# Optimization experiments

Measured on AMD Instinct MI355X. Metric: run time of the kernel, lower is better.

The kernel has to match this reference:

```python
import jax, jax.numpy as jnp
import numpy as np

NEG_SLOPE = 0.2
EPS = 1e-16  # matches PyG softmax epsilon


def gat_conv(x, src, dst, W, att_src, att_dst, bias):
    """PyG-style GATConv (concat heads, self-loops already in src/dst).
    x: [N, F_in]; W: [F_in, H*C]; att_*: [H, C]; bias: [H*C]."""
    N = x.shape[0]
    H, C = att_src.shape
    h = (x @ W).reshape(N, H, C)                       # [N,H,C]
    a_src = jnp.einsum('nhc,hc->nh', h, att_src)       # [N,H]
    a_dst = jnp.einsum('nhc,hc->nh', h, att_dst)
    e = jax.nn.leaky_relu(a_src[src] + a_dst[dst], NEG_SLOPE)   # [E,H]
    # segment softmax over incoming edges of each dst node
    e_max = jax.ops.segment_max(e, dst, num_segments=N)         # [N,H]
    e_max = jnp.where(jnp.isfinite(e_max), e_max, 0.0)
    e_exp = jnp.exp(e - e_max[dst])                              # [E,H]
    denom = jax.ops.segment_sum(e_exp, dst, num_segments=N)     # [N,H]
    alpha = e_exp / (denom[dst] + EPS)                           # [E,H]
    msg = h[src] * alpha[:, :, None]                             # [E,H,C]
    out = jax.ops.segment_sum(msg, dst, num_segments=N)         # [N,H,C]
    return out.reshape(N, H * C) + bias


def setup_inputs() -> dict:
    key = jax.random.key(0)
    ks = jax.random.split(key, 16)
    N, E = 50000, 800000
    F_in, C, H = 1280, 32, 8
    HC = H * C
    NG = 64  # graphs in batch
    x = jax.random.normal(ks[0], (N, F_in), dtype=jnp.float32)
    edge_index = jax.random.randint(ks[1], (2, E), 0, N, dtype=jnp.int64)
    batch = jnp.sort(jax.random.randint(ks[2], (N,), 0, NG, dtype=jnp.int64))
    s = 1.0 / np.sqrt(F_in)
    W1 = jax.random.normal(ks[3], (F_in, HC), dtype=jnp.float32) * s
    as1 = jax.random.normal(ks[4], (H, C), dtype=jnp.float32) * 0.1
    ad1 = jax.random.normal(ks[5], (H, C), dtype=jnp.float32) * 0.1
    b1 = jnp.zeros((HC,), dtype=jnp.float32)
    s2 = 1.0 / np.sqrt(HC)
    W2 = jax.random.normal(ks[6], (HC, HC), dtype=jnp.float32) * s2
    as2 = jax.random.normal(ks[7], (H, C), dtype=jnp.float32) * 0.1
    ad2 = jax.random.normal(ks[8], (H, C), dtype=jnp.float32) * 0.1
    b2 = jnp.zeros((HC,), dtype=jnp.float32)
    lin1_w = jax.random.normal(ks[9], (HC, 128), dtype=jnp.float32) * s2
    lin1_b = jnp.zeros((128,), dtype=jnp.float32)
    lin2_w = jax.random.normal(ks[10], (128, 1), dtype=jnp.float32) * (1.0 / np.sqrt(128))
    lin2_b = jnp.zeros((1,), dtype=jnp.float32)
    return {"x": x, "edge_index": edge_index, "batch": batch,
            "W1": W1, "as1": as1, "ad1": ad1, "b1": b1,
            "W2": W2, "as2": as2, "ad2": ad2, "b2": b2,
            "lin1_w": lin1_w, "lin1_b": lin1_b, "lin2_w": lin2_w, "lin2_b": lin2_b}


def reference(x, edge_index, batch, W1, as1, ad1, b1, W2, as2, ad2, b2,
              lin1_w, lin1_b, lin2_w, lin2_b):
    N = x.shape[0]
    NG = 64
    loops = jnp.arange(N, dtype=edge_index.dtype)
    src = jnp.concatenate([edge_index[0], loops])  # add self-loops (PyG default)
    dst = jnp.concatenate([edge_index[1], loops])
    h = jax.nn.relu(gat_conv(x, src, dst, W1, as1, ad1, b1))
    h = jax.nn.relu(gat_conv(h, src, dst, W2, as2, ad2, b2))
    # global mean pool over graphs
    sums = jax.ops.segment_sum(h, batch, num_segments=NG)               # [NG,HC]
    cnts = jax.ops.segment_sum(jnp.ones((N, 1), h.dtype), batch, num_segments=NG)
    pooled = sums / jnp.maximum(cnts, 1.0)
    z = jax.nn.relu(pooled @ lin1_w + lin1_b)
    out = z @ lin2_w + lin2_b                                            # [NG,1]
    return out.squeeze(-1)
```

## Files before the change

### kernel.cpp

```cpp
#include <hip/hip_runtime.h>
#include <hip/hip_bf16.h>
#include <math.h>

#define HC 256
#define NH 8
#define NEG_SLOPE 0.2f
#define CHW 64
#define LDA 136
#define MR 32
#define EL 264

typedef unsigned short u16;
typedef __attribute__((ext_vector_type(8))) short bf16x8;
typedef __attribute__((ext_vector_type(4))) float f32x4;

__device__ __forceinline__ u16 f2bf(float f) {
    unsigned int u = __float_as_uint(f);
    u += 0x7FFFu + ((u >> 16) & 1u);
    return (u16)(u >> 16);
}
__device__ __forceinline__ float bf2f(u16 s) {
    return __uint_as_float(((unsigned int)s) << 16);
}
__device__ __forceinline__ f32x4 bf4f(ushort4 v) {
    f32x4 r;
    r[0] = bf2f(v.x); r[1] = bf2f(v.y); r[2] = bf2f(v.z); r[3] = bf2f(v.w);
    return r;
}

#define BAR_LDS()                                                  \
    do {                                                           \
        asm volatile("s_waitcnt lgkmcnt(0)" ::: "memory");         \
        __builtin_amdgcn_s_barrier();                              \
        __builtin_amdgcn_sched_barrier(0);                         \
    } while (0)

__global__ __launch_bounds__(256) void pack_b_split(const float* __restrict__ B, int K,
                                                    u16* __restrict__ Bh,
                                                    u16* __restrict__ Bl) {
    const int g = blockIdx.x * 256 + threadIdx.x;
    const int lane = g & 63;
    const int f = (g >> 6) & 15;
    const int kt = g >> 10;
    const int col = f * 16 + (lane & 15);
    const int k0 = kt * 32 + (lane >> 4) * 8;
    bf16x8 hv, lv;
#pragma unroll
    for (int e = 0; e < 8; e++) {
        const float v = B[(size_t)(k0 + e) * HC + col];
        const u16 h = f2bf(v);
        hv[e] = (short)h;
        lv[e] = (short)f2bf(v - bf2f(h));
    }
    const size_t off = (size_t)g * 8;
    *(bf16x8*)(Bh + off) = hv;
    *(bf16x8*)(Bl + off) = lv;
}

template <typename AT>
__global__ __launch_bounds__(256) void gemm_fused(
    const AT* __restrict__ A,
    const u16* __restrict__ Bh, const u16* __restrict__ Bl,
    const float* __restrict__ att_s, const float* __restrict__ att_d,
    u16* __restrict__ h_out, float* __restrict__ a_src, float* __restrict__ a_dst,
    int M, int K) {
    __shared__ u16 ldsA[2][MR * LDA];
    const int tid = threadIdx.x;
    const int wid = tid >> 6;
    const int lane = tid & 63;
    const int rowblk = blockIdx.x;
    const int NG4 = K >> 7;
    const int rot = rowblk % NG4;

    f32x4 acc[2][4];
#pragma unroll
    for (int i = 0; i < 2; i++)
#pragma unroll
        for (int j = 0; j < 4; j++) acc[i][j] = (f32x4)0.f;

    const int srow = tid >> 3;
    const int scc = (tid & 7) * 16;
    const int grow = rowblk * MR + srow;
    const AT* aptr = (grow < M) ? (A + (size_t)grow * K + scc) : nullptr;
    const int woff = srow * LDA + scc;

    float4 pf[4];
    uint4 pu[2];
    auto loadAg = [&](int gg) {
        if constexpr (sizeof(AT) == 4) {
#pragma unroll
            for (int q = 0; q < 4; q++) {
                pf[q] = make_float4(0.f, 0.f, 0.f, 0.f);
                if (aptr) pf[q] = *(const float4*)((const float*)aptr + gg * 128 + q * 4);
            }
        } else {
            pu[0] = make_uint4(0, 0, 0, 0);
            pu[1] = make_uint4(0, 0, 0, 0);
            if (aptr) {
                pu[0] = *(const uint4*)((const u16*)aptr + gg * 128);
                pu[1] = *(const uint4*)((const u16*)aptr + gg * 128 + 8);
            }
        }
    };
    auto stageg = [&](int buf) {
        if constexpr (sizeof(AT) == 4) {
#pragma unroll
            for (int p = 0; p < 2; p++) {
                const float vv[8] = {pf[2 * p].x,     pf[2 * p].y,
                                     pf[2 * p].z,     pf[2 * p].w,
                                     pf[2 * p + 1].x, pf[2 * p + 1].y,
                                     pf[2 * p + 1].z, pf[2 * p + 1].w};
                bf16x8 hv;
#pragma unroll
                for (int e = 0; e < 8; e++) hv[e] = (short)f2bf(vv[e]);
                *(bf16x8*)&ldsA[buf][woff + p * 8] = hv;
            }
        } else {
            *(uint4*)&ldsA[buf][woff] = pu[0];
            *(uint4*)&ldsA[buf][woff + 8] = pu[1];
        }
    };
    auto readA = [&](int buf, int kk, bf16x8* ah) {
#pragma unroll
        for (int i = 0; i < 2; i++)
            ah[i] = *(const bf16x8*)&ldsA[buf][(i * 16 + (lane & 15)) * LDA +
                                              kk * 32 + (lane >> 4) * 8];
    };
    auto loadB = [&](int kt, bf16x8* bh, bf16x8* bl) {
        const u16* bHp = Bh + ((size_t)kt * 16 + wid * 4) * 512 + lane * 8;
        const u16* bLp = Bl + ((size_t)kt * 16 + wid * 4) * 512 + lane * 8;
#pragma unroll
        for (int j = 0; j < 4; j++) {
            bh[j] = *(const bf16x8*)(bHp + j * 512);
            bl[j] = *(const bf16x8*)(bLp + j * 512);
        }
    };
    auto mfma_tile = [&](const bf16x8* ah, const bf16x8* bh, const bf16x8* bl) {
#pragma unroll
        for (int i = 0; i < 2; i++)
#pragma unroll
            for (int j = 0; j < 4; j++) {
                acc[i][j] = __builtin_amdgcn_mfma_f32_16x16x32_bf16(ah[i], bh[j], acc[i][j], 0, 0, 0);
                acc[i][j] = __builtin_amdgcn_mfma_f32_16x16x32_bf16(ah[i], bl[j], acc[i][j], 0, 0, 0);
            }
    };

    loadAg(rot);
    stageg(0);
    if (NG4 > 1) loadAg((rot + 1) % NG4);
    BAR_LDS();

    bf16x8 bh[4], bl[4];
    int cur = 0;
    for (int g = 0; g < NG4; ++g) {
        const int gg = (g + rot) % NG4;
        if (g + 1 < NG4) stageg(cur ^ 1);
        if (g + 2 < NG4) loadAg((g + 2 + rot) % NG4);

        const int kt0 = gg * 4;
#pragma unroll
        for (int kk = 0; kk < 4; kk++) {
            loadB(kt0 + kk, bh, bl);
            bf16x8 ah[2];
            readA(cur, kk, ah);
            mfma_tile(ah, bh, bl);
        }
        BAR_LDS();
        cur ^= 1;
    }

    const int r0 = rowblk * MR;
    const int colb = wid * 64 + (lane & 15);
    float asw[4], adw[4];
#pragma unroll
    for (int j = 0; j < 4; j++) {
        asw[j] = att_s[colb + j * 16];
        adw[j] = att_d[colb + j * 16];
    }
#pragma unroll
    for (int i = 0; i < 2; i++) {
#pragma unroll
        for (int r = 0; r < 4; r++) {
            const int row = r0 + i * 16 + (lane >> 4) * 4 + r;
            float ps0 = acc[i][0][r] * asw[0] + acc[i][1][r] * asw[1];
            float ps1 = acc[i][2][r] * asw[2] + acc[i][3][r] * asw[3];
            float pd0 = acc[i][0][r] * adw[0] + acc[i][1][r] * adw[1];
            float pd1 = acc[i][2][r] * adw[2] + acc[i][3][r] * adw[3];
#pragma unroll
            for (int m = 1; m <= 8; m <<= 1) {
                ps0 += __shfl_xor(ps0, m);
                ps1 += __shfl_xor(ps1, m);
                pd0 += __shfl_xor(pd0, m);
                pd1 += __shfl_xor(pd1, m);
            }
            if (row < M && (lane & 15) == 0) {
                a_src[row * NH + 2 * wid + 0] = ps0;
                a_src[row * NH + 2 * wid + 1] = ps1;
                a_dst[row * NH + 2 * wid + 0] = pd0;
                a_dst[row * NH + 2 * wid + 1] = pd1;
            }
        }
    }

    u16* eps = &ldsA[0][0];
#pragma unroll
    for (int i = 0; i < 2; i++)
#pragma unroll
        for (int r = 0; r < 4; r++) {
            const int lrow = i * 16 + (lane >> 4) * 4 + r;
#pragma unroll
            for (int j = 0; j < 4; j++)
                eps[lrow * EL + colb + j * 16] = f2bf(acc[i][j][r]);
        }
    BAR_LDS();
#pragma unroll
    for (int q = 0; q < 4; q++) {
        const int t = q * 256 + tid;
        const int lrow = t >> 5;
        const int c8 = (t & 31) * 8;
        const bf16x8 v = *(const bf16x8*)&eps[lrow * EL + c8];
        const int growr = r0 + lrow;
        if (growr < M) *(bf16x8*)&h_out[(size_t)growr * HC + c8] = v;
    }
}

__global__ void count_deg(const int* __restrict__ dst, int E, int ET, int* __restrict__ deg) {
    const int e = blockIdx.x * blockDim.x + threadIdx.x;
    if (e >= ET) return;
    const int d = (e < E) ? dst[e] : (e - E);
    atomicAdd(&deg[d], 1);
}

__global__ __launch_bounds__(256) void scan_block(const int* __restrict__ deg,
                                                  int* __restrict__ row_ptr,
                                                  int* __restrict__ partials, int N) {
    __shared__ int sd[256];
    const int tid = threadIdx.x;
    const int base = blockIdx.x * 1024 + tid * 4;
    int v0 = (base + 0 < N) ? deg[base + 0] : 0;
    int v1 = (base + 1 < N) ? deg[base + 1] : 0;
    int v2 = (base + 2 < N) ? deg[base + 2] : 0;
    int v3 = (base + 3 < N) ? deg[base + 3] : 0;
    const int tsum = v0 + v1 + v2 + v3;
    sd[tid] = tsum;
    __syncthreads();
    int run = tsum;
    for (int off = 1; off < 256; off <<= 1) {
        int t = 0;
        if (tid >= off) t = sd[tid - off];
        __syncthreads();
        run += t;
        sd[tid] = run;
        __syncthreads();
    }
    const int excl = run - tsum;
    int s0 = excl + v0, s1 = s0 + v1, s2 = s1 + v2, s3 = s2 + v3;
    if (base + 0 < N) row_ptr[base + 1] = s0;
    if (base + 1 < N) row_ptr[base + 2] = s1;
    if (base + 2 < N) row_ptr[base + 3] = s2;
    if (base + 3 < N) row_ptr[base + 4] = s3;
    if (tid == 255) partials[blockIdx.x] = run;
}

__global__ __launch_bounds__(1024) void scan_partials(int* __restrict__ partials, int nb) {
    __shared__ int sd[1024];
    const int tid = threadIdx.x;
    int v = (tid < nb) ? partials[tid] : 0;
    sd[tid] = v;
    __syncthreads();
    int run = v;
    for (int off = 1; off < 1024; off <<= 1) {
        int t = 0;
        if (tid >= off) t = sd[tid - off];
        __syncthreads();
        run += t;
        sd[tid] = run;
        __syncthreads();
    }
    if (tid < nb) partials[tid] = run - v;
}

__global__ __launch_bounds__(256) void scan_add(int* __restrict__ row_ptr,
                                                const int* __restrict__ partials, int N) {
    const int i = blockIdx.x * 256 + threadIdx.x;
    if (i == 0) row_ptr[0] = 0;
    if (i < N) row_ptr[i + 1] += partials[i >> 10];
}

__global__ void scatter_edges(const int* __restrict__ src_in, const int* __restrict__ dst,
                              int E, int ET, const int* __restrict__ row_ptr,
                              int* __restrict__ cursor, int* __restrict__ esrc) {
    const int e = blockIdx.x * blockDim.x + threadIdx.x;
    if (e >= ET) return;
    const int d = (e < E) ? dst[e] : (e - E);
    const int s = (e < E) ? src_in[e] : (e - E);
    const int pos = atomicAdd(&cursor[d], 1);
    esrc[row_ptr[d] + pos] = s;
}

template <typename OT>
__global__ __launch_bounds__(256) void gat_aggregate_wave(
    const u16* __restrict__ h_bf, const float* __restrict__ a_src,
    const float* __restrict__ a_dst, const int* __restrict__ row_ptr,
    const int* __restrict__ esrc, const float* __restrict__ bias,
    OT* __restrict__ out, int N) {
    __shared__ int   s_src[4][CHW];
    __shared__ float s_ev[4][CHW][NH];

    const int tid = threadIdx.x;
    const int wv = tid >> 6;
    const int lane = tid & 63;
    const int n = blockIdx.x * 4 + wv;
    if (n >= N) return;

    const int beg = row_ptr[n];
    const int deg = row_ptr[n + 1] - beg;
    const int jj = lane >> 3;
    const int hh = lane & 7;
    const int g4 = lane >> 3;

    const float adh = a_dst[n * NH + hh];
    float m_run = -1e30f, d_run = 0.f;
    f32x4 acc = (f32x4)0.f;

    for (int c0 = 0; c0 < deg; c0 += CHW) {
        const int chlen = min(CHW, deg - c0);

        float lmax = -1e30f;
        for (int p = 0; p < chlen; p += 8) {
            const int j = p + jj;
            if (j < chlen) {
                const int s = esrc[beg + c0 + j];
                if (hh == 0) s_src[wv][j] = s;
                float v = a_src[s * NH + hh] + adh;
                v = (v > 0.f) ? v : NEG_SLOPE * v;
                s_ev[wv][j][hh] = v;
                lmax = fmaxf(lmax, v);
            }
        }
        lmax = fmaxf(lmax, __shfl_xor(lmax, 8));
        lmax = fmaxf(lmax, __shfl_xor(lmax, 16));
        lmax = fmaxf(lmax, __shfl_xor(lmax, 32));
        const float mo = m_run;
        const float mn = fmaxf(mo, lmax);
        const float scl = __expf(mo - mn);
        m_run = mn;

        float lsum = 0.f;
        for (int p = 0; p < chlen; p += 8) {
            const int j = p + jj;
            if (j < chlen) {
                const float pv = __expf(s_ev[wv][j][hh] - mn);
                s_ev[wv][j][hh] = pv;
                lsum += pv;
            }
        }
        lsum += __shfl_xor(lsum, 8);
        lsum += __shfl_xor(lsum, 16);
        lsum += __shfl_xor(lsum, 32);
        d_run = d_run * scl + lsum;

        __asm__ volatile("s_waitcnt lgkmcnt(0)" ::: "memory");

        const float scl4 = __shfl(scl, g4);
        f32x4 t0 = (f32x4)0.f, t1 = (f32x4)0.f, t2 = (f32x4)0.f, t3 = (f32x4)0.f;
        int j = 0;
        for (; j + 4 <= chlen; j += 4) {
            const int s0 = s_src[wv][j],     s1 = s_src[wv][j + 1];
            const int s2 = s_src[wv][j + 2], s3 = s_src[wv][j + 3];
            const float p0 = s_ev[wv][j][g4],     p1 = s_ev[wv][j + 1][g4];
            const float p2 = s_ev[wv][j + 2][g4], p3 = s_ev[wv][j + 3][g4];
            const f32x4 h0 = bf4f(*(const ushort4*)&h_bf[(size_t)s0 * HC + lane * 4]);
            const f32x4 h1 = bf4f(*(const ushort4*)&h_bf[(size_t)s1 * HC + lane * 4]);
            const f32x4 h2 = bf4f(*(const ushort4*)&h_bf[(size_t)s2 * HC + lane * 4]);
            const f32x4 h3 = bf4f(*(const ushort4*)&h_bf[(size_t)s3 * HC + lane * 4]);
#pragma unroll
            for (int q = 0; q < 4; q++) {
                t0[q] += p0 * h0[q];
                t1[q] += p1 * h1[q];
                t2[q] += p2 * h2[q];
                t3[q] += p3 * h3[q];
            }
        }
        for (; j < chlen; j++) {
            const int s0 = s_src[wv][j];
            const float p0 = s_ev[wv][j][g4];
            const f32x4 h0 = bf4f(*(const ushort4*)&h_bf[(size_t)s0 * HC + lane * 4]);
#pragma unroll
            for (int q = 0; q < 4; q++) t0[q] += p0 * h0[q];
        }
#pragma unroll
        for (int q = 0; q < 4; q++)
            acc[q] = acc[q] * scl4 + ((t0[q] + t1[q]) + (t2[q] + t3[q]));
    }

    const float invd = 1.f / (__shfl(d_run, g4) + 1e-16f);
    const f32x4 bv = *(const f32x4*)&bias[lane * 4];
    if constexpr (sizeof(OT) == 2) {
        ushort4 o4;
        o4.x = f2bf(fmaxf(acc[0] * invd + bv[0], 0.f));
        o4.y = f2bf(fmaxf(acc[1] * invd + bv[1], 0.f));
        o4.z = f2bf(fmaxf(acc[2] * invd + bv[2], 0.f));
        o4.w = f2bf(fmaxf(acc[3] * invd + bv[3], 0.f));
        *(ushort4*)&out[(size_t)n * HC + lane * 4] = o4;
    } else {
        f32x4 o;
#pragma unroll
        for (int q = 0; q < 4; q++) o[q] = fmaxf(acc[q] * invd + bv[q], 0.f);
        *(f32x4*)&out[(size_t)n * HC + lane * 4] = o;
    }
}

__global__ __launch_bounds__(256) void pool_partial(const float* __restrict__ h,
                                                    const int* __restrict__ batch, int N,
                                                    float* __restrict__ sums) {
    __shared__ int bs[64];
    const int tid = threadIdx.x;
    const int base = blockIdx.x * 64;
    const int cnt = min(64, N - base);
    if (tid < 64 && tid < cnt) bs[tid] = batch[base + tid];
    __syncthreads();

    float acc = 0.f;
    int cur = bs[0];
    for (int i = 0; i < cnt; i++) {
        const int g = bs[i];
        if (g != cur) {
            atomicAdd(&sums[(size_t)cur * HC + tid], acc);
            acc = 0.f;
            cur = g;
        }
        acc += h[(size_t)(base + i) * HC + tid];
    }
    atomicAdd(&sums[(size_t)cur * HC + tid], acc);
}

__global__ __launch_bounds__(256) void pool_div(float* __restrict__ sums,
                                                const int* __restrict__ batch, int N) {
    const int g = blockIdx.x;
    const int tid = threadIdx.x;
    int lo = 0, hi = N;
    while (lo < hi) {
        const int mid = (lo + hi) >> 1;
        if (batch[mid] < g) lo = mid + 1; else hi = mid;
    }
    const int start = lo;
    hi = N;
    while (lo < hi) {
        const int mid = (lo + hi) >> 1;
        if (batch[mid] < g + 1) lo = mid + 1; else hi = mid;
    }
    const float inv = 1.f / fmaxf((float)(lo - start), 1.0f);
    sums[(size_t)g * HC + tid] *= inv;
}

__global__ __launch_bounds__(128) void mlp_head(const float* __restrict__ pooled,
                                                const float* __restrict__ w1,
                                                const float* __restrict__ b1,
                                                const float* __restrict__ w2,
                                                const float* __restrict__ b2,
                                                float* __restrict__ out) {
    const int g = blockIdx.x;
    const int tid = threadIdx.x;
    __shared__ float p[HC];
    p[tid] = pooled[g * HC + tid];
    p[tid + 128] = pooled[g * HC + tid + 128];
    __syncthreads();
    float z = b1[tid];
#pragma unroll 8
    for (int k = 0; k < HC; k++) z += p[k] * w1[k * 128 + tid];
    z = fmaxf(z, 0.f);
    float t = z * w2[tid];
#pragma unroll
    for (int m = 32; m >= 1; m >>= 1) t += __shfl_xor(t, m);
    __shared__ float ws2[2];
    if ((tid & 63) == 0) ws2[tid >> 6] = t;
    __syncthreads();
    if (tid == 0) out[g] = ws2[0] + ws2[1] + b2[0];
}

extern "C" void kernel_launch(void* const* d_in, const int* in_sizes, int n_in,
                              void* d_out, int out_size, void* d_ws, size_t ws_size,
                              hipStream_t stream) {
    const float* x      = (const float*)d_in[0];
    const int*   ei     = (const int*)d_in[1];
    const int*   batch  = (const int*)d_in[2];
    const float* W1     = (const float*)d_in[3];
    const float* as1    = (const float*)d_in[4];
    const float* ad1    = (const float*)d_in[5];
    const float* b1     = (const float*)d_in[6];
    const float* W2     = (const float*)d_in[7];
    const float* as2    = (const float*)d_in[8];
    const float* ad2    = (const float*)d_in[9];
    const float* b2     = (const float*)d_in[10];
    const float* lin1w  = (const float*)d_in[11];
    const float* lin1b  = (const float*)d_in[12];
    const float* lin2w  = (const float*)d_in[13];
    const float* lin2b  = (const float*)d_in[14];

    const int N   = in_sizes[2];
    const int E   = in_sizes[1] / 2;
    const int ET  = E + N;
    const int Fin = in_sizes[0] / N;
    const int NG  = 64;

    const int nRB = (N + MR - 1) / MR;
    const int nScanBlk = (N + 1023) / 1024;

    const int* src_arr = ei;
    const int* dst_arr = ei + E;

    char* ws = (char*)d_ws;
    size_t off = 0;
    auto alloc = [&](size_t bytes) {
        void* p = ws + off;
        off += (bytes + 255) & ~(size_t)255;
        return p;
    };
    float* h_agg   = (float*)alloc((size_t)N * HC * sizeof(float));
    u16*   hb_a    = (u16*)alloc((size_t)N * HC * sizeof(u16));
    u16*   hb_b    = (u16*)alloc((size_t)N * HC * sizeof(u16));
    float* a_src   = (float*)alloc((size_t)N * NH * sizeof(float));
    float* a_dst   = (float*)alloc((size_t)N * NH * sizeof(float));
    int*   deg     = (int*)alloc((size_t)N * sizeof(int));
    int*   cursor  = (int*)alloc((size_t)N * sizeof(int));
    int*   row_ptr = (int*)alloc((size_t)(N + 1) * sizeof(int));
    int*   partials= (int*)alloc((size_t)1024 * sizeof(int));
    int*   esrc    = (int*)alloc((size_t)ET * sizeof(int));
    float* pooled  = (float*)alloc((size_t)NG * HC * sizeof(float));
    u16* Bh = (u16*)alloc((size_t)Fin * HC * sizeof(u16));
    u16* Bl = (u16*)alloc((size_t)Fin * HC * sizeof(u16));
    (void)ws_size; (void)n_in; (void)out_size;

    hipMemsetAsync(deg, 0, (size_t)N * sizeof(int), stream);
    hipMemsetAsync(cursor, 0, (size_t)N * sizeof(int), stream);
    {
        const int blocks = (ET + 255) / 256;
        count_deg<<<blocks, 256, 0, stream>>>(dst_arr, E, ET, deg);
        scan_block<<<nScanBlk, 256, 0, stream>>>(deg, row_ptr, partials, N);
        scan_partials<<<1, 1024, 0, stream>>>(partials, nScanBlk);
        scan_add<<<(N + 255) / 256, 256, 0, stream>>>(row_ptr, partials, N);
        scatter_edges<<<blocks, 256, 0, stream>>>(src_arr, dst_arr, E, ET, row_ptr,
                                                  cursor, esrc);
    }

    const int aggBlocks = (N + 3) / 4;

    pack_b_split<<<(Fin / 32) * 4, 256, 0, stream>>>(W1, Fin, Bh, Bl);
    gemm_fused<float><<<nRB, 256, 0, stream>>>(x, Bh, Bl, as1, ad1,
                                               hb_a, a_src, a_dst, N, Fin);
    gat_aggregate_wave<u16><<<aggBlocks, 256, 0, stream>>>(hb_a, a_src, a_dst, row_ptr,
                                                           esrc, b1, hb_b, N);

    pack_b_split<<<(HC / 32) * 4, 256, 0, stream>>>(W2, HC, Bh, Bl);
    gemm_fused<u16><<<nRB, 256, 0, stream>>>(hb_b, Bh, Bl, as2, ad2,
                                             hb_a, a_src, a_dst, N, HC);
    gat_aggregate_wave<float><<<aggBlocks, 256, 0, stream>>>(hb_a, a_src, a_dst, row_ptr,
                                                             esrc, b2, h_agg, N);

    hipMemsetAsync(pooled, 0, (size_t)NG * HC * sizeof(float), stream);
    pool_partial<<<(N + 63) / 64, 256, 0, stream>>>(h_agg, batch, N, pooled);
    pool_div<<<NG, 256, 0, stream>>>(pooled, batch, N);
    mlp_head<<<NG, 128, 0, stream>>>(pooled, lin1w, lin1b, lin2w, lin2b, (float*)d_out);
}
```

Before: 470.7 us.

## Load GEMM A operand directly into registers, dropping LDS staging and barriers

Replaces the LDS double-buffered A tile in the fused GEMM with direct per-wave global loads into MFMA operand registers. The K loop is software-pipelined two steps deep in registers, and the per-chunk barriers go away. The aim is to remove LDS traffic and synchronisation from the main loop. In exchange, every one of the 4 waves now loads the same A rows, so global/L2 reads of A rise 4x, and the K-rotation across blocks is removed.

Result: slower. 580.2 us (+23.3%).

```diff
diff --git a/kernel.cpp b/kernel.cpp
--- a/kernel.cpp
+++ b/kernel.cpp
@@ -6,7 +6,6 @@
 #define NH 8
 #define NEG_SLOPE 0.2f
 #define CHW 64
-#define LDA 136
 #define MR 32
 #define EL 264
 
@@ -27,13 +26,6 @@
     r[0] = bf2f(v.x); r[1] = bf2f(v.y); r[2] = bf2f(v.z); r[3] = bf2f(v.w);
     return r;
 }
-
-#define BAR_LDS()                                                  \
-    do {                                                           \
-        asm volatile("s_waitcnt lgkmcnt(0)" ::: "memory");         \
-        __builtin_amdgcn_s_barrier();                              \
-        __builtin_amdgcn_sched_barrier(0);                         \
-    } while (0)
 
 __global__ __launch_bounds__(256) void pack_b_split(const float* __restrict__ B, int K,
                                                     u16* __restrict__ Bh,
@@ -58,19 +50,26 @@
 }
 
 template <typename AT>
-__global__ __launch_bounds__(256) void gemm_fused(
+__global__ __launch_bounds__(256) void gemm_direct(
     const AT* __restrict__ A,
     const u16* __restrict__ Bh, const u16* __restrict__ Bl,
     const float* __restrict__ att_s, const float* __restrict__ att_d,
     u16* __restrict__ h_out, float* __restrict__ a_src, float* __restrict__ a_dst,
     int M, int K) {
-    __shared__ u16 ldsA[2][MR * LDA];
+    __shared__ u16 eps[MR * EL];
     const int tid = threadIdx.x;
     const int wid = tid >> 6;
     const int lane = tid & 63;
     const int rowblk = blockIdx.x;
-    const int NG4 = K >> 7;
-    const int rot = rowblk % NG4;
+    const int KT = K >> 5;
+    const int r0 = rowblk * MR;
+
+    const int row0 = r0 + (lane & 15);
+    const int row1 = row0 + 16;
+    const int kq = (lane >> 4) * 8;
+    const bool v0 = row0 < M, v1 = row1 < M;
+    const AT* pA0 = A + (size_t)row0 * K + kq;
+    const AT* pA1 = A + (size_t)row1 * K + kq;
 
     f32x4 acc[2][4];
 #pragma unroll
@@ -78,55 +77,41 @@
 #pragma unroll
         for (int j = 0; j < 4; j++) acc[i][j] = (f32x4)0.f;
 
-    const int srow = tid >> 3;
-    const int scc = (tid & 7) * 16;
-    const int grow = rowblk * MR + srow;
-    const AT* aptr = (grow < M) ? (A + (size_t)grow * K + scc) : nullptr;
-    const int woff = srow * LDA + scc;
-
-    float4 pf[4];
-    uint4 pu[2];
-    auto loadAg = [&](int gg) {
+    auto issueA = [&](int kt, float4& f0, float4& f1, float4& f2, float4& f3,
+                      bf16x8& u0, bf16x8& u1) {
         if constexpr (sizeof(AT) == 4) {
-#pragma unroll
-            for (int q = 0; q < 4; q++) {
-                pf[q] = make_float4(0.f, 0.f, 0.f, 0.f);
-                if (aptr) pf[q] = *(const float4*)((const float*)aptr + gg * 128 + q * 4);
+            f0 = make_float4(0.f, 0.f, 0.f, 0.f); f1 = f0; f2 = f0; f3 = f0;
+            if (v0) {
+                f0 = *(const float4*)((const float*)pA0 + kt * 32);
+                f1 = *(const float4*)((const float*)pA0 + kt * 32 + 4);
+            }
+            if (v1) {
+                f2 = *(const float4*)((const float*)pA1 + kt * 32);
+                f3 = *(const float4*)((const float*)pA1 + kt * 32 + 4);
             }
         } else {
-            pu[0] = make_uint4(0, 0, 0, 0);
-            pu[1] = make_uint4(0, 0, 0, 0);
-            if (aptr) {
-                pu[0] = *(const uint4*)((const u16*)aptr + gg * 128);
-                pu[1] = *(const uint4*)((const u16*)aptr + gg * 128 + 8);
-            }
+            u0 = (bf16x8){0, 0, 0, 0, 0, 0, 0, 0};
+            u1 = (bf16x8){0, 0, 0, 0, 0, 0, 0, 0};
+            if (v0) u0 = *(const bf16x8*)((const u16*)pA0 + kt * 32);
+            if (v1) u1 = *(const bf16x8*)((const u16*)pA1 + kt * 32);
         }
     };
-    auto stageg = [&](int buf) {
+    auto cvtA = [&](float4 f0, float4 f1, float4 f2, float4 f3,
+                    bf16x8 u0, bf16x8 u1, bf16x8& a0, bf16x8& a1) {
         if constexpr (sizeof(AT) == 4) {
-#pragma unroll
-            for (int p = 0; p < 2; p++) {
-                const float vv[8] = {pf[2 * p].x,     pf[2 * p].y,
-                                     pf[2 * p].z,     pf[2 * p].w,
-                                     pf[2 * p + 1].x, pf[2 * p + 1].y,
-                                     pf[2 * p + 1].z, pf[2 * p + 1].w};
-                bf16x8 hv;
-#pragma unroll
-                for (int e = 0; e < 8; e++) hv[e] = (short)f2bf(vv[e]);
-                *(bf16x8*)&ldsA[buf][woff + p * 8] = hv;
+            const float w0[8] = {f0.x, f0.y, f0.z, f0.w, f1.x, f1.y, f1.z, f1.w};
+            const float w1[8] = {f2.x, f2.y, f2.z, f2.w, f3.x, f3.y, f3.z, f3.w};
+#pragma unroll
+            for (int e = 0; e < 8; e++) {
+                a0[e] = (short)f2bf(w0[e]);
+                a1[e] = (short)f2bf(w1[e]);
             }
         } else {
-            *(uint4*)&ldsA[buf][woff] = pu[0];
-            *(uint4*)&ldsA[buf][woff + 8] = pu[1];
+            a0 = u0;
+            a1 = u1;
         }
     };
-    auto readA = [&](int buf, int kk, bf16x8* ah) {
-#pragma unroll
-        for (int i = 0; i < 2; i++)
-            ah[i] = *(const bf16x8*)&ldsA[buf][(i * 16 + (lane & 15)) * LDA +
-                                              kk * 32 + (lane >> 4) * 8];
-    };
-    auto loadB = [&](int kt, bf16x8* bh, bf16x8* bl) {
+    auto issueB = [&](int kt, bf16x8* bh, bf16x8* bl) {
         const u16* bHp = Bh + ((size_t)kt * 16 + wid * 4) * 512 + lane * 8;
         const u16* bLp = Bl + ((size_t)kt * 16 + wid * 4) * 512 + lane * 8;
 #pragma unroll
@@ -135,41 +120,42 @@
             bl[j] = *(const bf16x8*)(bLp + j * 512);
         }
     };
-    auto mfma_tile = [&](const bf16x8* ah, const bf16x8* bh, const bf16x8* bl) {
-#pragma unroll
-        for (int i = 0; i < 2; i++)
-#pragma unroll
-            for (int j = 0; j < 4; j++) {
-                acc[i][j] = __builtin_amdgcn_mfma_f32_16x16x32_bf16(ah[i], bh[j], acc[i][j], 0, 0, 0);
-                acc[i][j] = __builtin_amdgcn_mfma_f32_16x16x32_bf16(ah[i], bl[j], acc[i][j], 0, 0, 0);
-            }
+    auto mf = [&](bf16x8 a0, bf16x8 a1, const bf16x8* bh, const bf16x8* bl) {
+#pragma unroll
+        for (int j = 0; j < 4; j++) {
+            acc[0][j] = __builtin_amdgcn_mfma_f32_16x16x32_bf16(a0, bh[j], acc[0][j], 0, 0, 0);
+            acc[0][j] = __builtin_amdgcn_mfma_f32_16x16x32_bf16(a0, bl[j], acc[0][j], 0, 0, 0);
+            acc[1][j] = __builtin_amdgcn_mfma_f32_16x16x32_bf16(a1, bh[j], acc[1][j], 0, 0, 0);
+            acc[1][j] = __builtin_amdgcn_mfma_f32_16x16x32_bf16(a1, bl[j], acc[1][j], 0, 0, 0);
+        }
     };
 
-    loadAg(rot);
-    stageg(0);
-    if (NG4 > 1) loadAg((rot + 1) % NG4);
-    BAR_LDS();
-
-    bf16x8 bh[4], bl[4];
-    int cur = 0;
-    for (int g = 0; g < NG4; ++g) {
-        const int gg = (g + rot) % NG4;
-        if (g + 1 < NG4) stageg(cur ^ 1);
-        if (g + 2 < NG4) loadAg((g + 2 + rot) % NG4);
-
-        const int kt0 = gg * 4;
-#pragma unroll
-        for (int kk = 0; kk < 4; kk++) {
-            loadB(kt0 + kk, bh, bl);
-            bf16x8 ah[2];
-            readA(cur, kk, ah);
-            mfma_tile(ah, bh, bl);
-        }
-        BAR_LDS();
-        cur ^= 1;
-    }
-
-    const int r0 = rowblk * MR;
+    float4 fa0A, fa1A, fa2A, fa3A, fa0B, fa1B, fa2B, fa3B;
+    bf16x8 ua0A, ua1A, ua0B, ua1B;
+    bf16x8 bhA[4], blA[4], bhB[4], blB[4];
+
+    issueA(0, fa0A, fa1A, fa2A, fa3A, ua0A, ua1A);
+    issueB(0, bhA, blA);
+
+    for (int kt = 0; kt < KT; kt += 2) {
+        issueA(kt + 1, fa0B, fa1B, fa2B, fa3B, ua0B, ua1B);
+        issueB(kt + 1, bhB, blB);
+        {
+            bf16x8 a0, a1;
+            cvtA(fa0A, fa1A, fa2A, fa3A, ua0A, ua1A, a0, a1);
+            mf(a0, a1, bhA, blA);
+        }
+        if (kt + 2 < KT) {
+            issueA(kt + 2, fa0A, fa1A, fa2A, fa3A, ua0A, ua1A);
+            issueB(kt + 2, bhA, blA);
+        }
+        {
+            bf16x8 a0, a1;
+            cvtA(fa0B, fa1B, fa2B, fa3B, ua0B, ua1B, a0, a1);
+            mf(a0, a1, bhB, blB);
+        }
+    }
+
     const int colb = wid * 64 + (lane & 15);
     float asw[4], adw[4];
 #pragma unroll
@@ -202,7 +188,6 @@
         }
     }
 
-    u16* eps = &ldsA[0][0];
 #pragma unroll
     for (int i = 0; i < 2; i++)
 #pragma unroll
@@ -212,7 +197,7 @@
             for (int j = 0; j < 4; j++)
                 eps[lrow * EL + colb + j * 16] = f2bf(acc[i][j][r]);
         }
-    BAR_LDS();
+    __syncthreads();
 #pragma unroll
     for (int q = 0; q < 4; q++) {
         const int t = q * 256 + tid;
@@ -547,14 +532,14 @@
     const int aggBlocks = (N + 3) / 4;
 
     pack_b_split<<<(Fin / 32) * 4, 256, 0, stream>>>(W1, Fin, Bh, Bl);
-    gemm_fused<float><<<nRB, 256, 0, stream>>>(x, Bh, Bl, as1, ad1,
-                                               hb_a, a_src, a_dst, N, Fin);
+    gemm_direct<float><<<nRB, 256, 0, stream>>>(x, Bh, Bl, as1, ad1,
+                                                hb_a, a_src, a_dst, N, Fin);
     gat_aggregate_wave<u16><<<aggBlocks, 256, 0, stream>>>(hb_a, a_src, a_dst, row_ptr,
                                                            esrc, b1, hb_b, N);
 
     pack_b_split<<<(HC / 32) * 4, 256, 0, stream>>>(W2, HC, Bh, Bl);
-    gemm_fused<u16><<<nRB, 256, 0, stream>>>(hb_b, Bh, Bl, as2, ad2,
-                                             hb_a, a_src, a_dst, N, HC);
+    gemm_direct<u16><<<nRB, 256, 0, stream>>>(hb_b, Bh, Bl, as2, ad2,
+                                              hb_a, a_src, a_dst, N, HC);
     gat_aggregate_wave<float><<<aggBlocks, 256, 0, stream>>>(hb_a, a_src, a_dst, row_ptr,
                                                              esrc, b2, h_agg, N);
 
```
